# Optimization experiments

Measured on AMD Instinct MI355X. Metric: run time of the kernel, lower is better.

Reference implementation:

```python
import jax, jax.numpy as jnp
import numpy as np

T, E, D, I = 2048, 8, 1024, 2048

def setup_inputs() -> dict:
    key = jax.random.key(0)
    k1, k2, k3, k4, k5 = jax.random.split(key, 5)
    # kaiming_uniform_(a=2.236): bound = sqrt(6 / ((1 + a^2) * fan_in)); fan_in is dim -2 of the 3D param
    def kaiming(k, shape, fan_in):
        bound = np.sqrt(6.0 / ((1.0 + 2.236 ** 2) * fan_in))
        return jax.random.uniform(k, shape, jnp.float32, -bound, bound)
    return {
        "x": jax.random.normal(k1, (T, D), jnp.float32),
        "expert_indices": jax.random.randint(k2, (T,), 0, E, jnp.int32),
        "w_gate": kaiming(k3, (E, D, I), D),
        "w_up": kaiming(k4, (E, D, I), D),
        "w_down": kaiming(k5, (E, I, D), I),
    }

def reference(x, expert_indices, w_gate, w_up, w_down):
    # x: [T, D]; expert_indices: [T] in [0, E)
    onehot = jax.nn.one_hot(expert_indices, w_gate.shape[0], dtype=x.dtype)  # [T, E]
    # Compute all experts densely, then select per token (avoids materializing
    # a [T, D, I] gathered-weight tensor as the torch code does).
    gate = jnp.einsum('td,edi,te->ti', x, w_gate, onehot)   # [T, I]
    up = jnp.einsum('td,edi,te->ti', x, w_up, onehot)       # [T, I]
    hidden = jax.nn.silu(gate) * up                          # [T, I]
    out = jnp.einsum('ti,eid,te->td', hidden, w_down, onehot)  # [T, D]
    return out
```

## Files before the change

### kernel.cpp

```cpp
#include <hip/hip_runtime.h>
#include <hip/hip_bf16.h>


#define T_ 2048
#define E_ 8
#define D_ 1024
#define I_ 2048
#define BM 64
#define BN 64
#define BK 64
#define MAXRT ((T_ / BM) + E_)

typedef __attribute__((ext_vector_type(8))) __bf16 bf16x8;
typedef __attribute__((ext_vector_type(4))) float f32x4;
typedef __attribute__((ext_vector_type(4))) unsigned short us4;
typedef __attribute__((ext_vector_type(8))) unsigned short us8;

__device__ __forceinline__ unsigned short b16(float f) {
  __hip_bfloat16 h = __float2bfloat16(f);
  return *reinterpret_cast<unsigned short*>(&h);
}

__device__ __forceinline__ void gload16(const void* g, unsigned lds_addr) {
  __builtin_amdgcn_global_load_lds(
      (const __attribute__((address_space(1))) unsigned int*)(unsigned long long)g,
      (__attribute__((address_space(3))) unsigned int*)(unsigned long long)lds_addr,
      16, 0, 0);
}

__global__ void moe_count(const int* __restrict__ eidx, int* __restrict__ meta) {
  __shared__ int cnt[E_], cur[E_];
  const int tid = threadIdx.x;
  if (tid < E_) cnt[tid] = 0;
  __syncthreads();
  for (int t = tid; t < T_; t += 256) atomicAdd(&cnt[eidx[t]], 1);
  __syncthreads();
  if (tid == 0) {
    int s = 0;
    for (int i = 0; i < E_; ++i) {
      int c = cnt[i];
      meta[i] = c;
      meta[8 + i] = s;
      cur[i] = s;
      s += c;
    }
  }
  __syncthreads();
  for (int t = tid; t < T_; t += 256) {
    int e = eidx[t];
    int pp = atomicAdd(&cur[e], 1);
    meta[16 + pp] = t;
  }
}

__device__ __forceinline__ bool resolve_tile(const int* __restrict__ meta, int rt,
                                             int& e, int& row0, int& rows_valid) {
  int cum = 0;
  e = -1;
  row0 = 0;
  rows_valid = 0;
#pragma unroll
  for (int i = 0; i < E_; ++i) {
    int n = meta[i];
    int nt = (n + BM - 1) >> 6;
    if (e < 0 && rt < cum + nt) {
      e = i;
      int segS = meta[8 + i];
      row0 = segS + (rt - cum) * BM;
      int rv = segS + n - row0;
      rows_valid = rv > BM ? BM : rv;
    }
    cum += nt;
  }
  return e >= 0;
}


__global__ __launch_bounds__(256) void moe_gemm1(
    const float* __restrict__ x, const float* __restrict__ wg,
    const float* __restrict__ wu, const int* __restrict__ meta,
    __hip_bfloat16* __restrict__ hidden) {
  extern __shared__ char smem[];
  const int tid = threadIdx.x;
  const int lane = tid & 63;
  const int wv = tid >> 6;
  const int p = lane & 15, h = lane >> 4;

  int e, row0, rows_valid;
  if (!resolve_tile(meta, blockIdx.x, e, row0, rows_valid)) return;
  const int ct = blockIdx.y;
  const int* __restrict__ perm = meta + 16;

  const float* xp[2];
  unsigned lwA[2];
#pragma unroll
  for (int q = 0; q < 2; ++q) {
    const int s = q * 256 + tid;
    const int m = s >> 3, kb = s & 7;
    const int mm = m < rows_valid ? m : (rows_valid - 1);
    const int tok = perm[row0 + mm];
    xp[q] = x + (size_t)tok * D_ + kb * 8;
    lwA[q] = (unsigned)(m * 128 + ((kb ^ (m & 7)) * 16));
  }
  const float* wgp = wg + (size_t)e * D_ * I_ + (size_t)(ct * BN + lane);
  const float* wup = wu + (size_t)e * D_ * I_ + (size_t)(ct * BN + lane);
  unsigned lwB[4];
#pragma unroll
  for (int q = 0; q < 4; ++q) {
    const int kg = q * 4 + wv;
    lwB[q] = (unsigned)(lane * 128 + (((kg >> 1) ^ (lane & 7)) * 16) + (kg & 1) * 8);
  }

  unsigned offA[4][2], offB[2];
#pragma unroll
  for (int mf = 0; mf < 4; ++mf)
#pragma unroll
    for (int kk = 0; kk < 2; ++kk)
      offA[mf][kk] = (unsigned)((mf * 16 + p) * 128 + (((kk * 4 + h) ^ (p & 7)) * 16));
#pragma unroll
  for (int kk = 0; kk < 2; ++kk)
    offB[kk] = (unsigned)((wv * 16 + p) * 128 + (((kk * 4 + h) ^ (p & 7)) * 16));

  f32x4 accG[4], accU[4];
#pragma unroll
  for (int i = 0; i < 4; ++i) {
    accG[i] = f32x4{0.f, 0.f, 0.f, 0.f};
    accU[i] = f32x4{0.f, 0.f, 0.f, 0.f};
  }

  float4 ra[2], rb[2];
  float rg[4][4], ru[4][4];
  auto LOADT = [&](int kt) {
#pragma unroll
    for (int q = 0; q < 2; ++q) {
      ra[q] = *(const float4*)(xp[q] + kt * BK);
      rb[q] = *(const float4*)(xp[q] + kt * BK + 4);
    }
#pragma unroll
    for (int q = 0; q < 4; ++q) {
      const int kg = q * 4 + wv;
#pragma unroll
      for (int j = 0; j < 4; ++j) {
        const size_t ko = (size_t)(kt * BK + kg * 4 + j) * I_;
        rg[q][j] = wgp[ko];
        ru[q][j] = wup[ko];
      }
    }
  };
  auto WRITET = [&](unsigned base) {
#pragma unroll
    for (int q = 0; q < 2; ++q) {
      us8 v = {b16(ra[q].x), b16(ra[q].y), b16(ra[q].z), b16(ra[q].w),
               b16(rb[q].x), b16(rb[q].y), b16(rb[q].z), b16(rb[q].w)};
      *(us8*)(smem + base + lwA[q]) = v;
    }
#pragma unroll
    for (int q = 0; q < 4; ++q) {
      us4 vg = {b16(rg[q][0]), b16(rg[q][1]), b16(rg[q][2]), b16(rg[q][3])};
      us4 vu = {b16(ru[q][0]), b16(ru[q][1]), b16(ru[q][2]), b16(ru[q][3])};
      *(us4*)(smem + base + 8192u + lwB[q]) = vg;
      *(us4*)(smem + base + 16384u + lwB[q]) = vu;
    }
  };

  LOADT(0);
  WRITET(0);
  __syncthreads();
  const int KT = D_ / BK;
  for (int kt = 0; kt < KT; ++kt) {
    const unsigned cur = (unsigned)(kt & 1) * 24576u;
    if (kt + 1 < KT) LOADT(kt + 1);
#pragma unroll
    for (int kk = 0; kk < 2; ++kk) {
      bf16x8 aF[4];
#pragma unroll
      for (int mf = 0; mf < 4; ++mf)
        aF[mf] = *(const bf16x8*)(smem + cur + offA[mf][kk]);
      const bf16x8 bG = *(const bf16x8*)(smem + cur + 8192u + offB[kk]);
      const bf16x8 bU = *(const bf16x8*)(smem + cur + 16384u + offB[kk]);
#pragma unroll
      for (int mf = 0; mf < 4; ++mf) {
        accG[mf] = __builtin_amdgcn_mfma_f32_16x16x32_bf16(aF[mf], bG, accG[mf], 0, 0, 0);
        accU[mf] = __builtin_amdgcn_mfma_f32_16x16x32_bf16(aF[mf], bU, accU[mf], 0, 0, 0);
      }
    }
    if (kt + 1 < KT) WRITET(cur ^ 24576u);
    __syncthreads();
  }

  const int cbase = ct * BN + wv * 16 + p;
#pragma unroll
  for (int mf = 0; mf < 4; ++mf) {
#pragma unroll
    for (int j = 0; j < 4; ++j) {
      const int r = mf * 16 + h * 4 + j;
      if (r < rows_valid) {
        const float gv = accG[mf][j], uv = accU[mf][j];
        const float hv = gv / (1.f + __expf(-gv)) * uv;
        hidden[(size_t)(row0 + r) * I_ + cbase] = __float2bfloat16(hv);
      }
    }
  }
}

__global__ __launch_bounds__(256) void moe_gemm2(
    const __hip_bfloat16* __restrict__ hidden, const float* __restrict__ wd,
    const int* __restrict__ meta, float* __restrict__ out) {
  extern __shared__ char smem[];
  const int tid = threadIdx.x;
  const int lane = tid & 63;
  const int wv = tid >> 6;
  const int p = lane & 15, h = lane >> 4;

  int e, row0, rows_valid;
  if (!resolve_tile(meta, blockIdx.x, e, row0, rows_valid)) return;
  const int ct = blockIdx.y;
  const int* __restrict__ perm = meta + 16;

  size_t gAoff[2];
  unsigned lA[2];
#pragma unroll
  for (int q = 0; q < 2; ++q) {
    const int s = (wv + q * 4) * 64 + lane;
    const int m = s >> 3, pcb = s & 7;
    const int kblk = pcb ^ (m & 7);
    int mm = row0 + m;
    if (mm > T_ - 1) mm = T_ - 1;
    gAoff[q] = (size_t)mm * I_ + kblk * 8;
    lA[q] = (unsigned)(s * 16);
  }
  const float* wdp = wd + (size_t)e * I_ * D_ + (size_t)(ct * BN + lane);
  unsigned lwB[4];
#pragma unroll
  for (int q = 0; q < 4; ++q) {
    const int kg = q * 4 + wv;
    lwB[q] = (unsigned)(lane * 128 + (((kg >> 1) ^ (lane & 7)) * 16) + (kg & 1) * 8);
  }

  unsigned offA[4][2], offB[2];
#pragma unroll
  for (int mf = 0; mf < 4; ++mf)
#pragma unroll
    for (int kk = 0; kk < 2; ++kk)
      offA[mf][kk] = (unsigned)((mf * 16 + p) * 128 + (((kk * 4 + h) ^ (p & 7)) * 16));
#pragma unroll
  for (int kk = 0; kk < 2; ++kk)
    offB[kk] = (unsigned)((wv * 16 + p) * 128 + (((kk * 4 + h) ^ (p & 7)) * 16));

  f32x4 acc[4];
#pragma unroll
  for (int i = 0; i < 4; ++i) acc[i] = f32x4{0.f, 0.f, 0.f, 0.f};

  float rd[4][4];
  auto GLOADA = [&](unsigned base, int kt) {
#pragma unroll
    for (int q = 0; q < 2; ++q)
      gload16(hidden + gAoff[q] + kt * BK,
              (unsigned)(unsigned long long)(smem + base) + lA[q]);
  };
  auto LOADB = [&](int kt) {
#pragma unroll
    for (int q = 0; q < 4; ++q) {
      const int kg = q * 4 + wv;
#pragma unroll
      for (int j = 0; j < 4; ++j)
        rd[q][j] = wdp[(size_t)(kt * BK + kg * 4 + j) * D_];
    }
  };
  auto WRITEB = [&](unsigned base) {
#pragma unroll
    for (int q = 0; q < 4; ++q) {
      us4 v = {b16(rd[q][0]), b16(rd[q][1]), b16(rd[q][2]), b16(rd[q][3])};
      *(us4*)(smem + base + 8192u + lwB[q]) = v;
    }
  };

  GLOADA(0, 0);
  LOADB(0);
  WRITEB(0);
  __syncthreads();
  const int KT = I_ / BK;
  for (int kt = 0; kt < KT; ++kt) {
    const unsigned cur = (unsigned)(kt & 1) * 16384u;
    if (kt + 1 < KT) {
      GLOADA(cur ^ 16384u, kt + 1);
      LOADB(kt + 1);
    }
#pragma unroll
    for (int kk = 0; kk < 2; ++kk) {
      bf16x8 aF[4];
#pragma unroll
      for (int mf = 0; mf < 4; ++mf)
        aF[mf] = *(const bf16x8*)(smem + cur + offA[mf][kk]);
      const bf16x8 bB = *(const bf16x8*)(smem + cur + 8192u + offB[kk]);
#pragma unroll
      for (int mf = 0; mf < 4; ++mf)
        acc[mf] = __builtin_amdgcn_mfma_f32_16x16x32_bf16(aF[mf], bB, acc[mf], 0, 0, 0);
    }
    if (kt + 1 < KT) WRITEB(cur ^ 16384u);
    __syncthreads();
  }

  const int cbase = ct * BN + wv * 16 + p;
#pragma unroll
  for (int mf = 0; mf < 4; ++mf) {
#pragma unroll
    for (int j = 0; j < 4; ++j) {
      const int r = mf * 16 + h * 4 + j;
      if (r < rows_valid) {
        const int tok = perm[row0 + r];
        out[(size_t)tok * D_ + cbase] = acc[mf][j];
      }
    }
  }
}

extern "C" void kernel_launch(void* const* d_in, const int* in_sizes, int n_in,
                              void* d_out, int out_size, void* d_ws, size_t ws_size,
                              hipStream_t stream) {
  const float* x = (const float*)d_in[0];
  const int* eidx = (const int*)d_in[1];
  const float* wgate = (const float*)d_in[2];
  const float* wup = (const float*)d_in[3];
  const float* wdown = (const float*)d_in[4];
  float* out = (float*)d_out;

  int* meta = (int*)d_ws;
  __hip_bfloat16* hidden = (__hip_bfloat16*)((char*)d_ws + 65536);

  moe_count<<<dim3(1), dim3(256), 0, stream>>>(eidx, meta);
  moe_gemm1<<<dim3(MAXRT, I_ / BN), dim3(256), 48 * 1024, stream>>>(x, wgate, wup, meta, hidden);
  moe_gemm2<<<dim3(MAXRT, D_ / BN), dim3(256), 32 * 1024, stream>>>(hidden, wdown, meta, out);
}
```

Baseline: 316.1 us.

## Use 128-row tiles, pre-convert x to bf16, and transpose-read weight tiles via LDS

Doubles the M tile to 128 rows so each weight tile loaded from global memory is reused across twice as many tokens. A separate pre-pass converts x to bf16, which lets gemm1 stream activations straight into LDS with global_load_lds. Weight tiles are now fetched as coalesced float4 rows and read back transposed with ds_read_b64_tr_b16, replacing the scalar strided column loads. In exchange, LDS and register use per block grow, per-expert tile padding gets coarser, there is one extra kernel launch, and the inline asm waits on lgkmcnt(0) on every sub-step.

```diff
diff --git a/kernel.cpp b/kernel.cpp
--- a/kernel.cpp
+++ b/kernel.cpp
@@ -6,12 +6,13 @@
 #define E_ 8
 #define D_ 1024
 #define I_ 2048
-#define BM 64
+#define BM 128
 #define BN 64
 #define BK 64
 #define MAXRT ((T_ / BM) + E_)
 
 typedef __attribute__((ext_vector_type(8))) __bf16 bf16x8;
+typedef __attribute__((ext_vector_type(4))) __bf16 bf16x4;
 typedef __attribute__((ext_vector_type(4))) float f32x4;
 typedef __attribute__((ext_vector_type(4))) unsigned short us4;
 typedef __attribute__((ext_vector_type(8))) unsigned short us8;
@@ -26,6 +27,15 @@
       (const __attribute__((address_space(1))) unsigned int*)(unsigned long long)g,
       (__attribute__((address_space(3))) unsigned int*)(unsigned long long)lds_addr,
       16, 0, 0);
+}
+
+__global__ __launch_bounds__(256) void x_to_bf16(const float* __restrict__ x,
+                                                 __hip_bfloat16* __restrict__ xb) {
+  const int idx = blockIdx.x * 256 + threadIdx.x;
+  const float4* px = (const float4*)x;
+  const float4 a = px[idx * 2], b = px[idx * 2 + 1];
+  us8 v = {b16(a.x), b16(a.y), b16(a.z), b16(a.w), b16(b.x), b16(b.y), b16(b.z), b16(b.w)};
+  *(us8*)(xb + (size_t)idx * 8) = v;
 }
 
 __global__ void moe_count(const int* __restrict__ eidx, int* __restrict__ meta) {
@@ -62,7 +72,7 @@
 #pragma unroll
   for (int i = 0; i < E_; ++i) {
     int n = meta[i];
-    int nt = (n + BM - 1) >> 6;
+    int nt = (n + BM - 1) >> 7;
     if (e < 0 && rt < cum + nt) {
       e = i;
       int segS = meta[8 + i];
@@ -77,10 +87,10 @@
 
 
 __global__ __launch_bounds__(256) void moe_gemm1(
-    const float* __restrict__ x, const float* __restrict__ wg,
+    const __hip_bfloat16* __restrict__ xb, const float* __restrict__ wg,
     const float* __restrict__ wu, const int* __restrict__ meta,
     __hip_bfloat16* __restrict__ hidden) {
-  extern __shared__ char smem[];
+  __shared__ char smem[2 * 32768];
   const int tid = threadIdx.x;
   const int lane = tid & 63;
   const int wv = tid >> 6;
@@ -91,106 +101,115 @@
   const int ct = blockIdx.y;
   const int* __restrict__ perm = meta + 16;
 
-  const float* xp[2];
-  unsigned lwA[2];
-#pragma unroll
-  for (int q = 0; q < 2; ++q) {
+  const __hip_bfloat16* gA[4];
+  unsigned lAdst[4];
+#pragma unroll
+  for (int q = 0; q < 4; ++q) {
     const int s = q * 256 + tid;
-    const int m = s >> 3, kb = s & 7;
+    const int m = s >> 3, pcb = s & 7;
+    const int kblk = pcb ^ (m & 7);
     const int mm = m < rows_valid ? m : (rows_valid - 1);
     const int tok = perm[row0 + mm];
-    xp[q] = x + (size_t)tok * D_ + kb * 8;
-    lwA[q] = (unsigned)(m * 128 + ((kb ^ (m & 7)) * 16));
-  }
-  const float* wgp = wg + (size_t)e * D_ * I_ + (size_t)(ct * BN + lane);
-  const float* wup = wu + (size_t)e * D_ * I_ + (size_t)(ct * BN + lane);
-  unsigned lwB[4];
+    gA[q] = xb + (size_t)tok * D_ + kblk * 8;
+    lAdst[q] = (unsigned)(s * 16);
+  }
+  const float* wgb = wg + (size_t)e * D_ * I_;
+  const float* wub = wu + (size_t)e * D_ * I_;
+  size_t gBoff[4];
+  unsigned lB[4];
 #pragma unroll
   for (int q = 0; q < 4; ++q) {
-    const int kg = q * 4 + wv;
-    lwB[q] = (unsigned)(lane * 128 + (((kg >> 1) ^ (lane & 7)) * 16) + (kg & 1) * 8);
-  }
-
-  unsigned offA[4][2], offB[2];
-#pragma unroll
-  for (int mf = 0; mf < 4; ++mf)
+    const int s = q * 256 + tid;
+    const int k = s >> 4, fq = s & 15;
+    gBoff[q] = (size_t)k * I_ + (size_t)(ct * BN + fq * 4);
+    lB[q] = (unsigned)((k >> 2) * 512 + (fq >> 2) * 128 + (k & 3) * 32 + (fq & 3) * 8);
+  }
+  unsigned offA[8][2];
+#pragma unroll
+  for (int mf = 0; mf < 8; ++mf)
 #pragma unroll
     for (int kk = 0; kk < 2; ++kk)
       offA[mf][kk] = (unsigned)((mf * 16 + p) * 128 + (((kk * 4 + h) ^ (p & 7)) * 16));
+  unsigned trb[2];
 #pragma unroll
   for (int kk = 0; kk < 2; ++kk)
-    offB[kk] = (unsigned)((wv * 16 + p) * 128 + (((kk * 4 + h) ^ (p & 7)) * 16));
-
-  f32x4 accG[4], accU[4];
-#pragma unroll
-  for (int i = 0; i < 4; ++i) {
+    trb[kk] = (unsigned)(kk * 4096 + h * 1024 + wv * 128 + p * 8);
+  const unsigned ldsbase = (unsigned)(unsigned long long)smem;
+
+  f32x4 accG[8], accU[8];
+#pragma unroll
+  for (int i = 0; i < 8; ++i) {
     accG[i] = f32x4{0.f, 0.f, 0.f, 0.f};
     accU[i] = f32x4{0.f, 0.f, 0.f, 0.f};
   }
 
-  float4 ra[2], rb[2];
-  float rg[4][4], ru[4][4];
-  auto LOADT = [&](int kt) {
-#pragma unroll
-    for (int q = 0; q < 2; ++q) {
-      ra[q] = *(const float4*)(xp[q] + kt * BK);
-      rb[q] = *(const float4*)(xp[q] + kt * BK + 4);
-    }
+  float4 rg[4], ru[4];
+  auto LOADB = [&](int kt) {
 #pragma unroll
     for (int q = 0; q < 4; ++q) {
-      const int kg = q * 4 + wv;
-#pragma unroll
-      for (int j = 0; j < 4; ++j) {
-        const size_t ko = (size_t)(kt * BK + kg * 4 + j) * I_;
-        rg[q][j] = wgp[ko];
-        ru[q][j] = wup[ko];
+      const size_t o = (size_t)kt * BK * I_ + gBoff[q];
+      rg[q] = *(const float4*)(wgb + o);
+      ru[q] = *(const float4*)(wub + o);
+    }
+  };
+  auto WRITEB = [&](unsigned base) {
+#pragma unroll
+    for (int q = 0; q < 4; ++q) {
+      us4 vg = {b16(rg[q].x), b16(rg[q].y), b16(rg[q].z), b16(rg[q].w)};
+      us4 vu = {b16(ru[q].x), b16(ru[q].y), b16(ru[q].z), b16(ru[q].w)};
+      *(us4*)(smem + base + 16384u + lB[q]) = vg;
+      *(us4*)(smem + base + 24576u + lB[q]) = vu;
+    }
+  };
+  auto GLOADA = [&](unsigned base, int kt) {
+#pragma unroll
+    for (int q = 0; q < 4; ++q) gload16(gA[q] + kt * BK, ldsbase + base + lAdst[q]);
+  };
+  auto COMPUTE = [&](unsigned cur) {
+#pragma unroll
+    for (int kk = 0; kk < 2; ++kk) {
+      bf16x8 aF[8];
+#pragma unroll
+      for (int mf = 0; mf < 8; ++mf)
+        aF[mf] = *(const bf16x8*)(smem + cur + offA[mf][kk]);
+      const unsigned ag = ldsbase + cur + 16384u + trb[kk];
+      const unsigned au = ldsbase + cur + 24576u + trb[kk];
+      bf16x4 g0, g1, u0, u1;
+      asm volatile("ds_read_b64_tr_b16 %0, %1" : "=v"(g0) : "v"(ag));
+      asm volatile("ds_read_b64_tr_b16 %0, %1 offset:512" : "=v"(g1) : "v"(ag));
+      asm volatile("ds_read_b64_tr_b16 %0, %1" : "=v"(u0) : "v"(au));
+      asm volatile("ds_read_b64_tr_b16 %0, %1 offset:512" : "=v"(u1) : "v"(au));
+      asm volatile("s_waitcnt lgkmcnt(0)" ::: "memory");
+      __builtin_amdgcn_sched_barrier(0);
+      const bf16x8 bg = __builtin_shufflevector(g0, g1, 0, 1, 2, 3, 4, 5, 6, 7);
+      const bf16x8 bu = __builtin_shufflevector(u0, u1, 0, 1, 2, 3, 4, 5, 6, 7);
+#pragma unroll
+      for (int mf = 0; mf < 8; ++mf) {
+        accG[mf] = __builtin_amdgcn_mfma_f32_16x16x32_bf16(aF[mf], bg, accG[mf], 0, 0, 0);
+        accU[mf] = __builtin_amdgcn_mfma_f32_16x16x32_bf16(aF[mf], bu, accU[mf], 0, 0, 0);
       }
     }
   };
-  auto WRITET = [&](unsigned base) {
-#pragma unroll
-    for (int q = 0; q < 2; ++q) {
-      us8 v = {b16(ra[q].x), b16(ra[q].y), b16(ra[q].z), b16(ra[q].w),
-               b16(rb[q].x), b16(rb[q].y), b16(rb[q].z), b16(rb[q].w)};
-      *(us8*)(smem + base + lwA[q]) = v;
-    }
-#pragma unroll
-    for (int q = 0; q < 4; ++q) {
-      us4 vg = {b16(rg[q][0]), b16(rg[q][1]), b16(rg[q][2]), b16(rg[q][3])};
-      us4 vu = {b16(ru[q][0]), b16(ru[q][1]), b16(ru[q][2]), b16(ru[q][3])};
-      *(us4*)(smem + base + 8192u + lwB[q]) = vg;
-      *(us4*)(smem + base + 16384u + lwB[q]) = vu;
-    }
-  };
-
-  LOADT(0);
-  WRITET(0);
+
+  GLOADA(0, 0);
+  LOADB(0);
+  WRITEB(0);
   __syncthreads();
   const int KT = D_ / BK;
   for (int kt = 0; kt < KT; ++kt) {
-    const unsigned cur = (unsigned)(kt & 1) * 24576u;
-    if (kt + 1 < KT) LOADT(kt + 1);
-#pragma unroll
-    for (int kk = 0; kk < 2; ++kk) {
-      bf16x8 aF[4];
-#pragma unroll
-      for (int mf = 0; mf < 4; ++mf)
-        aF[mf] = *(const bf16x8*)(smem + cur + offA[mf][kk]);
-      const bf16x8 bG = *(const bf16x8*)(smem + cur + 8192u + offB[kk]);
-      const bf16x8 bU = *(const bf16x8*)(smem + cur + 16384u + offB[kk]);
-#pragma unroll
-      for (int mf = 0; mf < 4; ++mf) {
-        accG[mf] = __builtin_amdgcn_mfma_f32_16x16x32_bf16(aF[mf], bG, accG[mf], 0, 0, 0);
-        accU[mf] = __builtin_amdgcn_mfma_f32_16x16x32_bf16(aF[mf], bU, accU[mf], 0, 0, 0);
-      }
-    }
-    if (kt + 1 < KT) WRITET(cur ^ 24576u);
+    const unsigned cur = (unsigned)(kt & 1) * 32768u;
+    if (kt + 1 < KT) {
+      GLOADA(cur ^ 32768u, kt + 1);
+      LOADB(kt + 1);
+    }
+    COMPUTE(cur);
+    if (kt + 1 < KT) WRITEB(cur ^ 32768u);
     __syncthreads();
   }
 
   const int cbase = ct * BN + wv * 16 + p;
 #pragma unroll
-  for (int mf = 0; mf < 4; ++mf) {
+  for (int mf = 0; mf < 8; ++mf) {
 #pragma unroll
     for (int j = 0; j < 4; ++j) {
       const int r = mf * 16 + h * 4 + j;
@@ -206,7 +225,7 @@
 __global__ __launch_bounds__(256) void moe_gemm2(
     const __hip_bfloat16* __restrict__ hidden, const float* __restrict__ wd,
     const int* __restrict__ meta, float* __restrict__ out) {
-  extern __shared__ char smem[];
+  __shared__ char smem[2 * 24576];
   const int tid = threadIdx.x;
   const int lane = tid & 63;
   const int wv = tid >> 6;
@@ -217,62 +236,58 @@
   const int ct = blockIdx.y;
   const int* __restrict__ perm = meta + 16;
 
-  size_t gAoff[2];
-  unsigned lA[2];
-#pragma unroll
-  for (int q = 0; q < 2; ++q) {
-    const int s = (wv + q * 4) * 64 + lane;
+  const __hip_bfloat16* gA[4];
+  unsigned lAdst[4];
+#pragma unroll
+  for (int q = 0; q < 4; ++q) {
+    const int s = q * 256 + tid;
     const int m = s >> 3, pcb = s & 7;
     const int kblk = pcb ^ (m & 7);
-    int mm = row0 + m;
-    if (mm > T_ - 1) mm = T_ - 1;
-    gAoff[q] = (size_t)mm * I_ + kblk * 8;
-    lA[q] = (unsigned)(s * 16);
-  }
-  const float* wdp = wd + (size_t)e * I_ * D_ + (size_t)(ct * BN + lane);
-  unsigned lwB[4];
+    const int mm = row0 + (m < rows_valid ? m : (rows_valid - 1));
+    gA[q] = hidden + (size_t)mm * I_ + kblk * 8;
+    lAdst[q] = (unsigned)(s * 16);
+  }
+  const float* wdb = wd + (size_t)e * I_ * D_;
+  size_t gBoff[4];
+  unsigned lB[4];
 #pragma unroll
   for (int q = 0; q < 4; ++q) {
-    const int kg = q * 4 + wv;
-    lwB[q] = (unsigned)(lane * 128 + (((kg >> 1) ^ (lane & 7)) * 16) + (kg & 1) * 8);
-  }
-
-  unsigned offA[4][2], offB[2];
-#pragma unroll
-  for (int mf = 0; mf < 4; ++mf)
+    const int s = q * 256 + tid;
+    const int k = s >> 4, fq = s & 15;
+    gBoff[q] = (size_t)k * D_ + (size_t)(ct * BN + fq * 4);
+    lB[q] = (unsigned)((k >> 2) * 512 + (fq >> 2) * 128 + (k & 3) * 32 + (fq & 3) * 8);
+  }
+  unsigned offA[8][2];
+#pragma unroll
+  for (int mf = 0; mf < 8; ++mf)
 #pragma unroll
     for (int kk = 0; kk < 2; ++kk)
       offA[mf][kk] = (unsigned)((mf * 16 + p) * 128 + (((kk * 4 + h) ^ (p & 7)) * 16));
+  unsigned trb[2];
 #pragma unroll
   for (int kk = 0; kk < 2; ++kk)
-    offB[kk] = (unsigned)((wv * 16 + p) * 128 + (((kk * 4 + h) ^ (p & 7)) * 16));
-
-  f32x4 acc[4];
-#pragma unroll
-  for (int i = 0; i < 4; ++i) acc[i] = f32x4{0.f, 0.f, 0.f, 0.f};
-
-  float rd[4][4];
+    trb[kk] = (unsigned)(kk * 4096 + h * 1024 + wv * 128 + p * 8);
+  const unsigned ldsbase = (unsigned)(unsigned long long)smem;
+
+  f32x4 acc[8];
+#pragma unroll
+  for (int i = 0; i < 8; ++i) acc[i] = f32x4{0.f, 0.f, 0.f, 0.f};
+
+  float4 rd[4];
+  auto LOADB = [&](int kt) {
+#pragma unroll
+    for (int q = 0; q < 4; ++q) rd[q] = *(const float4*)(wdb + (size_t)kt * BK * D_ + gBoff[q]);
+  };
+  auto WRITEB = [&](unsigned base) {
+#pragma unroll
+    for (int q = 0; q < 4; ++q) {
+      us4 v = {b16(rd[q].x), b16(rd[q].y), b16(rd[q].z), b16(rd[q].w)};
+      *(us4*)(smem + base + 16384u + lB[q]) = v;
+    }
+  };
   auto GLOADA = [&](unsigned base, int kt) {
 #pragma unroll
-    for (int q = 0; q < 2; ++q)
-      gload16(hidden + gAoff[q] + kt * BK,
-              (unsigned)(unsigned long long)(smem + base) + lA[q]);
-  };
-  auto LOADB = [&](int kt) {
-#pragma unroll
-    for (int q = 0; q < 4; ++q) {
-      const int kg = q * 4 + wv;
-#pragma unroll
-      for (int j = 0; j < 4; ++j)
-        rd[q][j] = wdp[(size_t)(kt * BK + kg * 4 + j) * D_];
-    }
-  };
-  auto WRITEB = [&](unsigned base) {
-#pragma unroll
-    for (int q = 0; q < 4; ++q) {
-      us4 v = {b16(rd[q][0]), b16(rd[q][1]), b16(rd[q][2]), b16(rd[q][3])};
-      *(us4*)(smem + base + 8192u + lwB[q]) = v;
-    }
+    for (int q = 0; q < 4; ++q) gload16(gA[q] + kt * BK, ldsbase + base + lAdst[q]);
   };
 
   GLOADA(0, 0);
@@ -281,29 +296,35 @@
   __syncthreads();
   const int KT = I_ / BK;
   for (int kt = 0; kt < KT; ++kt) {
-    const unsigned cur = (unsigned)(kt & 1) * 16384u;
+    const unsigned cur = (unsigned)(kt & 1) * 24576u;
     if (kt + 1 < KT) {
-      GLOADA(cur ^ 16384u, kt + 1);
+      GLOADA(cur ^ 24576u, kt + 1);
       LOADB(kt + 1);
     }
 #pragma unroll
     for (int kk = 0; kk < 2; ++kk) {
-      bf16x8 aF[4];
-#pragma unroll
-      for (int mf = 0; mf < 4; ++mf)
+      bf16x8 aF[8];
+#pragma unroll
+      for (int mf = 0; mf < 8; ++mf)
         aF[mf] = *(const bf16x8*)(smem + cur + offA[mf][kk]);
-      const bf16x8 bB = *(const bf16x8*)(smem + cur + 8192u + offB[kk]);
-#pragma unroll
-      for (int mf = 0; mf < 4; ++mf)
-        acc[mf] = __builtin_amdgcn_mfma_f32_16x16x32_bf16(aF[mf], bB, acc[mf], 0, 0, 0);
-    }
-    if (kt + 1 < KT) WRITEB(cur ^ 16384u);
+      const unsigned ab = ldsbase + cur + 16384u + trb[kk];
+      bf16x4 b0, b1;
+      asm volatile("ds_read_b64_tr_b16 %0, %1" : "=v"(b0) : "v"(ab));
+      asm volatile("ds_read_b64_tr_b16 %0, %1 offset:512" : "=v"(b1) : "v"(ab));
+      asm volatile("s_waitcnt lgkmcnt(0)" ::: "memory");
+      __builtin_amdgcn_sched_barrier(0);
+      const bf16x8 bb = __builtin_shufflevector(b0, b1, 0, 1, 2, 3, 4, 5, 6, 7);
+#pragma unroll
+      for (int mf = 0; mf < 8; ++mf)
+        acc[mf] = __builtin_amdgcn_mfma_f32_16x16x32_bf16(aF[mf], bb, acc[mf], 0, 0, 0);
+    }
+    if (kt + 1 < KT) WRITEB(cur ^ 24576u);
     __syncthreads();
   }
 
   const int cbase = ct * BN + wv * 16 + p;
 #pragma unroll
-  for (int mf = 0; mf < 4; ++mf) {
+  for (int mf = 0; mf < 8; ++mf) {
 #pragma unroll
     for (int j = 0; j < 4; ++j) {
       const int r = mf * 16 + h * 4 + j;
@@ -326,9 +347,11 @@
   float* out = (float*)d_out;
 
   int* meta = (int*)d_ws;
-  __hip_bfloat16* hidden = (__hip_bfloat16*)((char*)d_ws + 65536);
-
+  __hip_bfloat16* xb = (__hip_bfloat16*)((char*)d_ws + 65536);
+  __hip_bfloat16* hidden = (__hip_bfloat16*)((char*)d_ws + 4259840);
+
+  x_to_bf16<<<dim3((T_ * D_) / (256 * 8)), dim3(256), 0, stream>>>(x, xb);
   moe_count<<<dim3(1), dim3(256), 0, stream>>>(eidx, meta);
-  moe_gemm1<<<dim3(MAXRT, I_ / BN), dim3(256), 48 * 1024, stream>>>(x, wgate, wup, meta, hidden);
-  moe_gemm2<<<dim3(MAXRT, D_ / BN), dim3(256), 32 * 1024, stream>>>(hidden, wdown, meta, out);
-}
+  moe_gemm1<<<dim3(MAXRT, I_ / BN), dim3(256), 0, stream>>>(xb, wgate, wup, meta, hidden);
+  moe_gemm2<<<dim3(MAXRT, D_ / BN), dim3(256), 0, stream>>>(hidden, wdown, meta, out);
+}
```

After: 343.0 us. 1.09x slower.
